# Performance work log

Measured on AMD Instinct MI355X. Metric: run time of the kernel, lower is better.

The kernel has to match this reference:

```python
import jax, jax.numpy as jnp
import numpy as np
from jax import lax

G, K, KS = 4, 16, 3            # stripes, latents per stripe, support kernel
TEMP, TOPK_RATIO, GATE, EPS = 0.125, 0.125, 0.05, 1e-6


def _l2norm(v):
    # F.normalize(p=2, dim=-1): divide by max(norm, 1e-12)
    return v / jnp.maximum(jnp.linalg.norm(v, axis=-1, keepdims=True), 1e-12)


def _avg_pool3(x):
    # 3x3 avg pool, stride 1, pad 1, count_include_pad=True (torch default)
    s = lax.reduce_window(x, 0.0, lax.add, (1, 1, KS, KS), (1, 1, 1, 1),
                          [(0, 0), (0, 0), (KS // 2, KS // 2), (KS // 2, KS // 2)])
    return s / float(KS * KS)


def setup_inputs() -> dict:
    key = jax.random.key(0)
    k1, k2 = jax.random.split(key)
    x = jax.random.normal(k1, (64, 256, 64, 44), dtype=jnp.float32)
    latent_basis = jax.random.normal(k2, (G, K, 256), dtype=jnp.float32) * 0.05
    return {"x": x, "latent_basis": latent_basis}


def reference(x, latent_basis):
    n, c, h, w = x.shape
    hs = h // G
    # 'n c (g hs) w -> (n g) c hs w'
    sf = x.reshape(n, c, G, hs, w).transpose(0, 2, 1, 3, 4).reshape(n * G, c, hs, w)
    support_feat = _avg_pool3(sf)
    feat_flat = sf.reshape(n, G, c, hs * w).transpose(0, 1, 3, 2)          # n g p c
    supp_flat = support_feat.reshape(n, G, c, hs * w).transpose(0, 1, 3, 2)  # n g p c
    # active mask from detached energy
    e = jnp.mean(lax.stop_gradient(sf) ** 2, axis=1)                       # [n*G, hs, w]
    e = e / jnp.maximum(jnp.max(e, axis=(-2, -1), keepdims=True), EPS)
    am = (e > GATE).astype(jnp.float32)
    fb = (e > 0).astype(jnp.float32)
    use_fb = jnp.sum(am, axis=(-2, -1), keepdims=True) <= 0
    am = jnp.where(use_fb, fb, am).reshape(n, G, hs * w)                   # n g p
    # routing
    sfn = _l2norm(supp_flat)
    lb = _l2norm(latent_basis)                                             # g k c
    logits = jnp.einsum('ngpc,gkc->ngpk', sfn, lb) / TEMP
    route = jax.nn.softmax(logits, axis=-1)
    supp = route * am[..., None]                                           # n g p k
    pw = supp / jnp.maximum(jnp.sum(supp, axis=2, keepdims=True), EPS)
    tokens = jnp.einsum('ngpk,ngpc->ngkc', pw, feat_flat)                  # n g k c
    tokens = tokens.transpose(0, 3, 1, 2).reshape(n, c, G * K)             # n c (g k)
    # presence via top-k over positions
    p = supp.shape[2]
    topk = max(1, min(p, int(p * TOPK_RATIO)))
    vals = lax.top_k(supp.transpose(0, 1, 3, 2), topk)[0]                  # n g k topk
    pres = jnp.mean(vals, axis=-1).reshape(n, G * K)
    pres = pres / jnp.maximum(jnp.sum(pres, axis=1, keepdims=True), EPS)
    return tokens, pres
```

## Files before the change

kernel.cpp:

```cpp
#include <hip/hip_runtime.h>
#include <cstdint>


#define C_ 256
#define W_ 44
#define P_ 704
#define CH_STRIDE 2816
#define NB_STRIDE 720896
#define TOPK_ 88
#define GATE_ 0.05f
#define EPS_ 1e-6f

#define DPP_WAVE_SHL1 0x130
#define DPP_WAVE_SHR1 0x138
__device__ __forceinline__ float dpp_from_left(float v) {
  return __int_as_float(__builtin_amdgcn_update_dpp(
      0, __float_as_int(v), DPP_WAVE_SHR1, 0xF, 0xF, true));
}
__device__ __forceinline__ float dpp_from_right(float v) {
  return __int_as_float(__builtin_amdgcn_update_dpp(
      0, __float_as_int(v), DPP_WAVE_SHL1, 0xF, 0xF, true));
}

__global__ __launch_bounds__(256) void k_norm_basis(const float* __restrict__ lb,
                                                    float* __restrict__ lbn) {
  int gk = blockIdx.x;
  int t = threadIdx.x;
  float v = lb[gk * 256 + t];
  float ss = v * v;
  #pragma unroll
  for (int off = 32; off >= 1; off >>= 1) ss += __shfl_xor(ss, off);
  __shared__ float red[4];
  if ((t & 63) == 0) red[t >> 6] = ss;
  __syncthreads();
  float tot = red[0] + red[1] + red[2] + red[3];
  float scale = 1.f / fmaxf(sqrtf(tot), 1e-12f);
  int g = gk >> 4, k = gk & 15;
  lbn[((g * 256 + t) << 4) + k] = v * scale;
}

#define LOAD_GRP(Pm, P0, Pp, cbase)                                    \
  { _Pragma("unroll")                                                  \
    for (int j_ = 0; j_ < 4; j_++) {                                   \
      const size_t o_ = (size_t)((cbase) + j_) * CH_STRIDE;            \
      Pm[j_] = xm[o_]; P0[j_] = xb[o_]; Pp[j_] = xp[o_];               \
    } }

#define CONS_GRP(Pm, P0, Pp, cbase)                                    \
  { _Pragma("unroll")                                                  \
    for (int j_ = 0; j_ < 4; j_++) {                                   \
      float a  = act ? P0[j_] : 0.f;                                   \
      float am_ = (act && hm) ? Pm[j_] : 0.f;                          \
      float ap_ = (act && hp) ? Pp[j_] : 0.f;                          \
      float vs = am_ + a + ap_;                                        \
      float lf = dpp_from_left(vs);                                    \
      float rt = dpp_from_right(vs);                                   \
      float win = lf + vs + rt;                                        \
      pw2 = fmaf(win, win, pw2);                                       \
      sq  = fmaf(a, a, sq);                                            \
      const int co_ = __builtin_amdgcn_readfirstlane(((cbase) + j_) << 4); \
      const float4* wp4 = (const float4*)(lbb + co_);                  \
      float4 w0 = wp4[0], w1 = wp4[1], w2 = wp4[2], w3 = wp4[3];       \
      rawdot[0]  = fmaf(a, w0.x, rawdot[0]);  rawdot[1]  = fmaf(a, w0.y, rawdot[1]);  \
      rawdot[2]  = fmaf(a, w0.z, rawdot[2]);  rawdot[3]  = fmaf(a, w0.w, rawdot[3]);  \
      rawdot[4]  = fmaf(a, w1.x, rawdot[4]);  rawdot[5]  = fmaf(a, w1.y, rawdot[5]);  \
      rawdot[6]  = fmaf(a, w1.z, rawdot[6]);  rawdot[7]  = fmaf(a, w1.w, rawdot[7]);  \
      rawdot[8]  = fmaf(a, w2.x, rawdot[8]);  rawdot[9]  = fmaf(a, w2.y, rawdot[9]);  \
      rawdot[10] = fmaf(a, w2.z, rawdot[10]); rawdot[11] = fmaf(a, w2.w, rawdot[11]); \
      rawdot[12] = fmaf(a, w3.x, rawdot[12]); rawdot[13] = fmaf(a, w3.y, rawdot[13]); \
      rawdot[14] = fmaf(a, w3.z, rawdot[14]); rawdot[15] = fmaf(a, w3.w, rawdot[15]); \
    } }

__global__ __launch_bounds__(256, 4) void k_route_dot(const float* __restrict__ x,
                                                      const float* __restrict__ lbn,
                                                      float* __restrict__ pd0,
                                                      float* __restrict__ pd1,
                                                      float* __restrict__ sqpw) {
  const int tid = threadIdx.x;
  const int wq = tid >> 6;
  const int l = tid & 63;
  const bool act = (l < 44);
  const int bid = blockIdx.x;
  const int s = bid >> 3;
  const int rem = bid & 7;
  const int q = rem >> 1, half = rem & 1;
  const int w = q * 4 + wq;
  const int n = s >> 2, g = s & 3;
  const int p = w * 44 + l;

  const int lsafe = act ? l : 0;
  const float* xb = x + (size_t)n * NB_STRIDE + (size_t)(half * 128) * CH_STRIDE
                      + (g * 16 + w) * 44 + lsafe;
  const float* xm = xb + ((w > 0)  ? -44 : 0);
  const float* xp = xb + ((w < 15) ?  44 : 0);
  const bool hm = (w > 0), hp = (w < 15);

  const float* lbb = lbn + (g << 12) + (half << 11);

  float rawdot[16];
  #pragma unroll
  for (int k = 0; k < 16; k++) rawdot[k] = 0.f;
  float sq = 0.f, pw2 = 0.f;

  float Avm[4], Av0[4], Avp[4];
  float Bvm[4], Bv0[4], Bvp[4];

  LOAD_GRP(Avm, Av0, Avp, 0)
  for (int c = 0; c < 128; c += 8) {
    LOAD_GRP(Bvm, Bv0, Bvp, c + 4)
    CONS_GRP(Avm, Av0, Avp, c)
    if (c + 8 < 128) { LOAD_GRP(Avm, Av0, Avp, c + 8) }
    CONS_GRP(Bvm, Bv0, Bvp, c + 4)
  }

  if (act) {
    float* dst = (half ? pd1 : pd0) + (size_t)s * 11264 + p * 16;
    #pragma unroll
    for (int kq = 0; kq < 4; kq++)
      ((float4*)dst)[kq] = make_float4(rawdot[kq*4+0], rawdot[kq*4+1],
                                       rawdot[kq*4+2], rawdot[kq*4+3]);
    *(float2*)(sqpw + ((size_t)(s * 2 + half) * 704 + p) * 2) = make_float2(sq, pw2);
  }
}

__global__ __launch_bounds__(1024) void k_route_fin(const float* __restrict__ pd0,
                                                    const float* __restrict__ pd1,
                                                    const float* __restrict__ sqpw,
                                                    float* __restrict__ supp_pk,
                                                    float* __restrict__ invden_ws,
                                                    float* __restrict__ presraw) {
  __shared__ float rsl[11264];
  __shared__ uint32_t hist_l[16 * 256];
  __shared__ float redA[16];
  __shared__ float redB[16];
  __shared__ float redM[2];
  __shared__ float red2[16 * 16];

  const int tid = threadIdx.x;
  const int w = tid >> 6;
  const int l = tid & 63;
  const bool act = (l < 44);
  const int s = blockIdx.x;
  const int p = w * 44 + l;

  float sq = 0.f, pw2 = 0.f;
  if (act) {
    const float4* a0 = (const float4*)(pd0 + (size_t)s * 11264 + p * 16);
    const float4* a1 = (const float4*)(pd1 + (size_t)s * 11264 + p * 16);
    #pragma unroll
    for (int kq = 0; kq < 4; kq++) {
      float4 u = a0[kq], v = a1[kq];
      rsl[(kq*4+0) * 704 + p] = u.x + v.x;
      rsl[(kq*4+1) * 704 + p] = u.y + v.y;
      rsl[(kq*4+2) * 704 + p] = u.z + v.z;
      rsl[(kq*4+3) * 704 + p] = u.w + v.w;
    }
    float2 s0 = *(const float2*)(sqpw + ((size_t)(s * 2 + 0) * 704 + p) * 2);
    float2 s1 = *(const float2*)(sqpw + ((size_t)(s * 2 + 1) * 704 + p) * 2);
    sq = s0.x + s1.x; pw2 = s0.y + s1.y;
  }
  __syncthreads();

  float pd[16];
  #pragma unroll
  for (int k = 0; k < 16; k++) pd[k] = 0.f;
  if (act) {
    #pragma unroll
    for (int dy = -1; dy <= 1; dy++) {
      int yy = w + dy;
      if (yy < 0 || yy > 15) continue;
      #pragma unroll
      for (int dx = -1; dx <= 1; dx++) {
        int xx = l + dx;
        if (xx < 0 || xx > 43) continue;
        int pp = yy * 44 + xx;
        #pragma unroll
        for (int k = 0; k < 16; k++) pd[k] += rsl[k * 704 + pp];
      }
    }
  }

  float e_raw = sq * (1.f / 256.f);
  float m = e_raw;
  #pragma unroll
  for (int off = 32; off >= 1; off >>= 1) m = fmaxf(m, __shfl_xor(m, off));
  if (l == 0) redA[w] = m;
  __syncthreads();
  if (tid == 0) {
    float mm = redA[0];
    for (int w2 = 1; w2 < 16; w2++) mm = fmaxf(mm, redA[w2]);
    redM[0] = mm;
  }
  __syncthreads();
  float M = fmaxf(redM[0], EPS_);
  float e = e_raw / M;
  float am = (e > GATE_) ? 1.f : 0.f;
  float fb = (e_raw > 0.f) ? 1.f : 0.f;
  float a = am;
  #pragma unroll
  for (int off = 32; off >= 1; off >>= 1) a += __shfl_xor(a, off);
  if (l == 0) redB[w] = a;
  __syncthreads();
  if (tid == 0) {
    float sm = 0.f;
    for (int w2 = 0; w2 < 16; w2++) sm += redB[w2];
    redM[1] = sm;
  }
  __syncthreads();
  if (redM[1] <= 0.f) am = fb;

  float pnorm = sqrtf(pw2) * (1.f / 9.f);
  float invn = 1.f / fmaxf(pnorm, 1e-12f);
  float scl = invn * (8.f / 9.f);
  float li[16];
  float mx = -1e30f;
  #pragma unroll
  for (int k = 0; k < 16; k++) { li[k] = pd[k] * scl; mx = fmaxf(mx, li[k]); }
  float ssum = 0.f;
  #pragma unroll
  for (int k = 0; k < 16; k++) { li[k] = __expf(li[k] - mx); ssum += li[k]; }
  float rs2 = am / ssum;
  float supp[16];
  #pragma unroll
  for (int k = 0; k < 16; k++) supp[k] = li[k] * rs2;

  if (act) {
    float* spk = supp_pk + ((size_t)s * 704 + p) * 16;
    #pragma unroll
    for (int kq = 0; kq < 4; kq++)
      ((float4*)spk)[kq] = make_float4(supp[kq*4+0], supp[kq*4+1],
                                       supp[kq*4+2], supp[kq*4+3]);
  }

  #pragma unroll
  for (int k = 0; k < 16; k++) {
    float v2 = act ? supp[k] : 0.f;
    #pragma unroll
    for (int off = 32; off >= 1; off >>= 1) v2 += __shfl_xor(v2, off);
    if (l == 0) red2[w * 16 + k] = v2;
  }
  __syncthreads();
  if (tid < 16) {
    float den = 0.f;
    for (int w2 = 0; w2 < 16; w2++) den += red2[w2 * 16 + tid];
    invden_ws[s * 16 + tid] = 1.f / fmaxf(den, EPS_);
  }

  if (act) {
    #pragma unroll
    for (int k = 0; k < 16; k++) rsl[k * 704 + p] = supp[k];
  }
  __syncthreads();

  {
    const int k = w;
    uint32_t key[11];
    #pragma unroll
    for (int j = 0; j < 11; j++)
      key[j] = __float_as_uint(rsl[k * 704 + l + 64 * j]);
    uint32_t* h = &hist_l[w * 256];
    uint32_t prefix = 0, remaining = TOPK_;
    #pragma unroll
    for (int b = 3; b >= 0; b--) {
      const int shift = b * 8;
      *(uint4*)&h[l * 4] = make_uint4(0u, 0u, 0u, 0u);
      uint32_t mhi = (b == 3) ? 0u : (0xFFFFFFFFu << (shift + 8));
      #pragma unroll
      for (int j = 0; j < 11; j++)
        if ((key[j] & mhi) == (prefix & mhi))
          atomicAdd(&h[(key[j] >> shift) & 255u], 1u);
      uint4 bn = *(uint4*)&h[l * 4];
      uint32_t T = bn.x + bn.y + bn.z + bn.w;
      uint32_t inc = T;
      #pragma unroll
      for (int off = 1; off < 64; off <<= 1) {
        uint32_t o = (uint32_t)__shfl_down((int)inc, off);
        if (l + off < 64) inc += o;
      }
      uint32_t excl = inc - T;
      uint32_t g3 = excl + bn.w, g2 = g3 + bn.z, g1 = g2 + bn.y, g0 = g1 + bn.x;
      uint32_t pk = 0u;
      if (g0 >= remaining && g1 < remaining) pk = ((uint32_t)(4*l+0) << 16) | (remaining - g1);
      if (g1 >= remaining && g2 < remaining) pk = ((uint32_t)(4*l+1) << 16) | (remaining - g2);
      if (g2 >= remaining && g3 < remaining) pk = ((uint32_t)(4*l+2) << 16) | (remaining - g3);
      if (g3 >= remaining && excl < remaining) pk = ((uint32_t)(4*l+3) << 16) | (remaining - excl);
      #pragma unroll
      for (int off = 32; off >= 1; off >>= 1) pk |= (uint32_t)__shfl_xor((int)pk, off);
      prefix |= ((pk >> 16) & 255u) << shift;
      remaining = pk & 0xFFFFu;
    }
    float tf = __uint_as_float(prefix);
    float sgt = 0.f; uint32_t cgt = 0u;
    #pragma unroll
    for (int j = 0; j < 11; j++)
      if (key[j] > prefix) { sgt += __uint_as_float(key[j]); cgt++; }
    #pragma unroll
    for (int off = 32; off >= 1; off >>= 1) {
      sgt += __shfl_xor(sgt, off);
      cgt += (uint32_t)__shfl_xor((int)cgt, off);
    }
    if (l == 0)
      presraw[s * 16 + k] = (sgt + (float)(TOPK_ - cgt) * tf) * (1.f / (float)TOPK_);
  }
}

__global__ __launch_bounds__(512, 4) void k_tokens(const float* __restrict__ x,
                                                   const float* __restrict__ supp_pk,
                                                   const float* __restrict__ invden,
                                                   float* __restrict__ out) {
  __shared__ float xl[4096];
  const int tid = threadIdx.x;
  const int bid = blockIdx.x;
  const int s = bid >> 1, chalf = bid & 1;
  const int n = s >> 2, g = s & 3;
  const int cl = tid & 127;
  const int q = tid >> 7;
  const int sblk = s * (704 * 16);

  const float* xs = x + (size_t)n * NB_STRIDE + (size_t)(chalf * 128) * CH_STRIDE + g * P_;

  const int li0 = tid, li1 = tid + 512;
  const int lc0 = li0 >> 3, lj0 = li0 & 7;
  const int lc1 = li1 >> 3, lj1 = li1 & 7;
  const float* gp0 = xs + (size_t)lc0 * CH_STRIDE + lj0 * 4;
  const float* gp1 = xs + (size_t)lc1 * CH_STRIDE + lj1 * 4;
  const int wo0 = lc0 * 32 + ((lj0 * 4) ^ ((lc0 & 7) * 4));
  const int wo1 = lc1 * 32 + ((lj1 * 4) ^ ((lc1 & 7) * 4));

  const int sw = (cl & 7) * 4;
  const int rbase = cl * 32;

  float acc[16];
  #pragma unroll
  for (int k = 0; k < 16; k++) acc[k] = 0.f;

  float4 r0 = *(const float4*)gp0;
  float4 r1 = *(const float4*)gp1;
  *(float4*)&xl[wo0] = r0;
  *(float4*)&xl[wo1] = r1;
  __syncthreads();

  for (int tt = 0; tt < 22; tt++) {
    const int p0 = tt * 32;
    float4 n0, n1;
    if (tt < 21) {
      n0 = *(const float4*)(gp0 + p0 + 32);
      n1 = *(const float4*)(gp1 + p0 + 32);
    }

    #pragma unroll
    for (int jj = 0; jj < 8; jj += 4) {
      const int pp0 = q * 8 + jj;
      float4 xv = *(const float4*)&xl[rbase + (pp0 ^ sw)];
      float xa[4] = {xv.x, xv.y, xv.z, xv.w};
      #pragma unroll
      for (int dj = 0; dj < 4; dj++) {
        int uofs = __builtin_amdgcn_readfirstlane(sblk + (p0 + pp0 + dj) * 16);
        const float4* sp = (const float4*)(supp_pk + uofs);
        float4 s0 = sp[0], s1 = sp[1], s2 = sp[2], s3 = sp[3];
        float a = xa[dj];
        acc[0]  += a * s0.x; acc[1]  += a * s0.y; acc[2]  += a * s0.z; acc[3]  += a * s0.w;
        acc[4]  += a * s1.x; acc[5]  += a * s1.y; acc[6]  += a * s1.z; acc[7]  += a * s1.w;
        acc[8]  += a * s2.x; acc[9]  += a * s2.y; acc[10] += a * s2.z; acc[11] += a * s2.w;
        acc[12] += a * s3.x; acc[13] += a * s3.y; acc[14] += a * s3.z; acc[15] += a * s3.w;
      }
    }

    __syncthreads();
    if (tt < 21) {
      *(float4*)&xl[wo0] = n0;
      *(float4*)&xl[wo1] = n1;
      __syncthreads();
    }
  }

  if (q >= 2) {
    float* dst = &xl[((q - 2) * 128 + cl) * 16];
    #pragma unroll
    for (int kq = 0; kq < 4; kq++)
      ((float4*)dst)[kq] = make_float4(acc[kq*4], acc[kq*4+1], acc[kq*4+2], acc[kq*4+3]);
  }
  __syncthreads();
  if (q < 2) {
    const float* src = &xl[(q * 128 + cl) * 16];
    #pragma unroll
    for (int k = 0; k < 16; k++) acc[k] += src[k];
  }
  __syncthreads();
  if (q == 1) {
    float* dst = &xl[cl * 16];
    #pragma unroll
    for (int kq = 0; kq < 4; kq++)
      ((float4*)dst)[kq] = make_float4(acc[kq*4], acc[kq*4+1], acc[kq*4+2], acc[kq*4+3]);
  }
  __syncthreads();
  if (q == 0) {
    const float* src = &xl[cl * 16];
    float* op = out + ((size_t)(n * 256 + chalf * 128 + cl) * 64) + g * 16;
    #pragma unroll
    for (int kq = 0; kq < 4; kq++) {
      int u = __builtin_amdgcn_readfirstlane(s * 16 + kq * 4);
      const float4 iv = *(const float4*)(invden + u);
      float4 o;
      o.x = (acc[kq*4+0] + src[kq*4+0]) * iv.x;
      o.y = (acc[kq*4+1] + src[kq*4+1]) * iv.y;
      o.z = (acc[kq*4+2] + src[kq*4+2]) * iv.z;
      o.w = (acc[kq*4+3] + src[kq*4+3]) * iv.w;
      ((float4*)op)[kq] = o;
    }
  }
}

__global__ __launch_bounds__(64) void k_pres(const float* __restrict__ presraw,
                                             float* __restrict__ out) {
  const int n = blockIdx.x, t = threadIdx.x;
  float v = presraw[n * 64 + t];
  float ssum = v;
  #pragma unroll
  for (int off = 32; off >= 1; off >>= 1) ssum += __shfl_xor(ssum, off);
  out[1048576 + n * 64 + t] = v / fmaxf(ssum, EPS_);
}

extern "C" void kernel_launch(void* const* d_in, const int* in_sizes, int n_in,
                              void* d_out, int out_size, void* d_ws, size_t ws_size,
                              hipStream_t stream) {
  (void)in_sizes; (void)n_in; (void)out_size; (void)ws_size;
  const float* x  = (const float*)d_in[0];
  const float* lb = (const float*)d_in[1];
  float* out = (float*)d_out;
  float* ws = (float*)d_ws;
  float* lbn_ws     = ws;
  float* invden_ws  = ws + 16384;
  float* presraw_ws = ws + 20480;
  float* supp_kp_ws = ws + 24576;
  float* supp_pk_ws = ws + 2908160;
  float* sqpw_ws    = out;

  k_norm_basis<<<64, 256, 0, stream>>>(lb, lbn_ws);
  k_route_dot<<<2048, 256, 0, stream>>>(x, lbn_ws, supp_kp_ws, supp_pk_ws, sqpw_ws);
  k_route_fin<<<256, 1024, 0, stream>>>(supp_kp_ws, supp_pk_ws, sqpw_ws,
                                        supp_pk_ws, invden_ws, presraw_ws);
  k_tokens<<<512, 512, 0, stream>>>(x, supp_pk_ws, invden_ws, out);
  k_pres<<<64, 64, 0, stream>>>(presraw_ws, out);
}
```

Baseline: 345.7 us.

## Pack positions densely across wave lanes in route_dot with halo lanes

Changes k_route_dot's lane-to-position mapping. Each 64-lane wave now covers 62 consecutive flattened positions plus halo lanes, instead of one 44-wide row with 20 idle lanes. Row boundaries inside a wave are handled by masking the DPP neighbour values at columns 0 and 43, and the grid shrinks from 2048 to 1536 blocks. The aim is to cut wasted lanes and the redundant loads and FMAs they cause. In exchange it adds per-lane modulo arithmetic and unaligned loads that straddle rows, and the last wave is only partly used.

```diff
diff --git a/kernel.cpp b/kernel.cpp
--- a/kernel.cpp
+++ b/kernel.cpp
@@ -53,8 +53,8 @@
       float am_ = (act && hm) ? Pm[j_] : 0.f;                          \
       float ap_ = (act && hp) ? Pp[j_] : 0.f;                          \
       float vs = am_ + a + ap_;                                        \
-      float lf = dpp_from_left(vs);                                    \
-      float rt = dpp_from_right(vs);                                   \
+      float lf = dpp_from_left(vs);  lf = coln0  ? lf : 0.f;           \
+      float rt = dpp_from_right(vs); rt = coln43 ? rt : 0.f;           \
       float win = lf + vs + rt;                                        \
       pw2 = fmaf(win, win, pw2);                                       \
       sq  = fmaf(a, a, sq);                                            \
@@ -79,21 +79,25 @@
   const int tid = threadIdx.x;
   const int wq = tid >> 6;
   const int l = tid & 63;
-  const bool act = (l < 44);
   const int bid = blockIdx.x;
-  const int s = bid >> 3;
-  const int rem = bid & 7;
+  const int s = bid / 6;
+  const int rem = bid % 6;
   const int q = rem >> 1, half = rem & 1;
-  const int w = q * 4 + wq;
+  const int wv = q * 4 + wq;
   const int n = s >> 2, g = s & 3;
-  const int p = w * 44 + l;
-
-  const int lsafe = act ? l : 0;
+  const int p = wv * 62 + l;
+  const int psafe = (p <= 703) ? p : 703;
+  const int col = psafe % 44;
+  const bool act = (p <= 703);
+  const bool own = (l >= 1 && l <= 62 && p <= 703) || (wv == 0 && l == 0);
+  const bool hm = (psafe >= 44);
+  const bool hp = (psafe <= 659);
+  const bool coln0 = (col != 0), coln43 = (col != 43);
+
   const float* xb = x + (size_t)n * NB_STRIDE + (size_t)(half * 128) * CH_STRIDE
-                      + (g * 16 + w) * 44 + lsafe;
-  const float* xm = xb + ((w > 0)  ? -44 : 0);
-  const float* xp = xb + ((w < 15) ?  44 : 0);
-  const bool hm = (w > 0), hp = (w < 15);
+                      + g * 704 + psafe;
+  const float* xm = xb + (hm ? -44 : 0);
+  const float* xp = xb + (hp ?  44 : 0);
 
   const float* lbb = lbn + (g << 12) + (half << 11);
 
@@ -113,13 +117,13 @@
     CONS_GRP(Bvm, Bv0, Bvp, c + 4)
   }
 
-  if (act) {
-    float* dst = (half ? pd1 : pd0) + (size_t)s * 11264 + p * 16;
+  if (own) {
+    float* dst = (half ? pd1 : pd0) + (size_t)s * 11264 + psafe * 16;
     #pragma unroll
     for (int kq = 0; kq < 4; kq++)
       ((float4*)dst)[kq] = make_float4(rawdot[kq*4+0], rawdot[kq*4+1],
                                        rawdot[kq*4+2], rawdot[kq*4+3]);
-    *(float2*)(sqpw + ((size_t)(s * 2 + half) * 704 + p) * 2) = make_float2(sq, pw2);
+    *(float2*)(sqpw + ((size_t)(s * 2 + half) * 704 + psafe) * 2) = make_float2(sq, pw2);
   }
 }
 
@@ -437,7 +441,7 @@
   float* sqpw_ws    = out;
 
   k_norm_basis<<<64, 256, 0, stream>>>(lb, lbn_ws);
-  k_route_dot<<<2048, 256, 0, stream>>>(x, lbn_ws, supp_kp_ws, supp_pk_ws, sqpw_ws);
+  k_route_dot<<<1536, 256, 0, stream>>>(x, lbn_ws, supp_kp_ws, supp_pk_ws, sqpw_ws);
   k_route_fin<<<256, 1024, 0, stream>>>(supp_kp_ws, supp_pk_ws, sqpw_ws,
                                         supp_pk_ws, invden_ws, presraw_ws);
   k_tokens<<<512, 512, 0, stream>>>(x, supp_pk_ws, invden_ws, out);
```

New measurement: 345.3 us. Within noise of the previous version (-0.1%).

## Register-block four rows per wave in route_dot to reuse halo loads

Applied to the files above, without the earlier changes.

Each wave now computes four consecutive image rows instead of one, loading six rows per channel (the four rows plus one halo row on each side) instead of three loads per output row. This removes the redundant vertical-halo reloads and amortizes each basis-weight load over four rows. The grid shrinks from 2048 to 512 blocks, and per-thread accumulators grow to 64 dot products, so launch bounds are relaxed to 2 waves/SIMD. The risks are higher register pressure, lower occupancy and fewer blocks to hide memory latency.

```diff
diff --git a/kernel.cpp b/kernel.cpp
--- a/kernel.cpp
+++ b/kernel.cpp
@@ -39,39 +39,40 @@
   lbn[((g * 256 + t) << 4) + k] = v * scale;
 }
 
-#define LOAD_GRP(Pm, P0, Pp, cbase)                                    \
-  { _Pragma("unroll")                                                  \
+#define LOAD6(R, cbase)                                                \
+  { const size_t o_ = (size_t)(cbase) * CH_STRIDE;                     \
+    R[0] = rp0[o_]; R[1] = rp1[o_]; R[2] = rp2[o_];                    \
+    R[3] = rp3[o_]; R[4] = rp4[o_]; R[5] = rp5[o_]; }
+
+#define CONS6(R, cbase)                                                \
+  { const int co_ = __builtin_amdgcn_readfirstlane((cbase) << 4);      \
+    const float4* wp4 = (const float4*)(lbb + co_);                    \
+    float4 w0 = wp4[0], w1 = wp4[1], w2 = wp4[2], w3 = wp4[3];         \
+    _Pragma("unroll")                                                  \
     for (int j_ = 0; j_ < 4; j_++) {                                   \
-      const size_t o_ = (size_t)((cbase) + j_) * CH_STRIDE;            \
-      Pm[j_] = xm[o_]; P0[j_] = xb[o_]; Pp[j_] = xp[o_];               \
-    } }
-
-#define CONS_GRP(Pm, P0, Pp, cbase)                                    \
-  { _Pragma("unroll")                                                  \
-    for (int j_ = 0; j_ < 4; j_++) {                                   \
-      float a  = act ? P0[j_] : 0.f;                                   \
-      float am_ = (act && hm) ? Pm[j_] : 0.f;                          \
-      float ap_ = (act && hp) ? Pp[j_] : 0.f;                          \
+      float a  = act ? R[j_ + 1] : 0.f;                                \
+      bool hmj = (j_ > 0) || hmw;                                      \
+      bool hpj = (j_ < 3) || hpw;                                      \
+      float am_ = (act && hmj) ? R[j_] : 0.f;                          \
+      float ap_ = (act && hpj) ? R[j_ + 2] : 0.f;                      \
       float vs = am_ + a + ap_;                                        \
       float lf = dpp_from_left(vs);                                    \
       float rt = dpp_from_right(vs);                                   \
       float win = lf + vs + rt;                                        \
-      pw2 = fmaf(win, win, pw2);                                       \
-      sq  = fmaf(a, a, sq);                                            \
-      const int co_ = __builtin_amdgcn_readfirstlane(((cbase) + j_) << 4); \
-      const float4* wp4 = (const float4*)(lbb + co_);                  \
-      float4 w0 = wp4[0], w1 = wp4[1], w2 = wp4[2], w3 = wp4[3];       \
-      rawdot[0]  = fmaf(a, w0.x, rawdot[0]);  rawdot[1]  = fmaf(a, w0.y, rawdot[1]);  \
-      rawdot[2]  = fmaf(a, w0.z, rawdot[2]);  rawdot[3]  = fmaf(a, w0.w, rawdot[3]);  \
-      rawdot[4]  = fmaf(a, w1.x, rawdot[4]);  rawdot[5]  = fmaf(a, w1.y, rawdot[5]);  \
-      rawdot[6]  = fmaf(a, w1.z, rawdot[6]);  rawdot[7]  = fmaf(a, w1.w, rawdot[7]);  \
-      rawdot[8]  = fmaf(a, w2.x, rawdot[8]);  rawdot[9]  = fmaf(a, w2.y, rawdot[9]);  \
-      rawdot[10] = fmaf(a, w2.z, rawdot[10]); rawdot[11] = fmaf(a, w2.w, rawdot[11]); \
-      rawdot[12] = fmaf(a, w3.x, rawdot[12]); rawdot[13] = fmaf(a, w3.y, rawdot[13]); \
-      rawdot[14] = fmaf(a, w3.z, rawdot[14]); rawdot[15] = fmaf(a, w3.w, rawdot[15]); \
+      pw2[j_] = fmaf(win, win, pw2[j_]);                               \
+      sq[j_]  = fmaf(a, a, sq[j_]);                                    \
+      float* rd = &rawdot[j_][0];                                      \
+      rd[0]  = fmaf(a, w0.x, rd[0]);  rd[1]  = fmaf(a, w0.y, rd[1]);   \
+      rd[2]  = fmaf(a, w0.z, rd[2]);  rd[3]  = fmaf(a, w0.w, rd[3]);   \
+      rd[4]  = fmaf(a, w1.x, rd[4]);  rd[5]  = fmaf(a, w1.y, rd[5]);   \
+      rd[6]  = fmaf(a, w1.z, rd[6]);  rd[7]  = fmaf(a, w1.w, rd[7]);   \
+      rd[8]  = fmaf(a, w2.x, rd[8]);  rd[9]  = fmaf(a, w2.y, rd[9]);   \
+      rd[10] = fmaf(a, w2.z, rd[10]); rd[11] = fmaf(a, w2.w, rd[11]);  \
+      rd[12] = fmaf(a, w3.x, rd[12]); rd[13] = fmaf(a, w3.y, rd[13]);  \
+      rd[14] = fmaf(a, w3.z, rd[14]); rd[15] = fmaf(a, w3.w, rd[15]);  \
     } }
 
-__global__ __launch_bounds__(256, 4) void k_route_dot(const float* __restrict__ x,
+__global__ __launch_bounds__(256, 2) void k_route_dot(const float* __restrict__ x,
                                                       const float* __restrict__ lbn,
                                                       float* __restrict__ pd0,
                                                       float* __restrict__ pd1,
@@ -81,45 +82,53 @@
   const int l = tid & 63;
   const bool act = (l < 44);
   const int bid = blockIdx.x;
-  const int s = bid >> 3;
-  const int rem = bid & 7;
-  const int q = rem >> 1, half = rem & 1;
-  const int w = q * 4 + wq;
+  const int s = bid >> 1, half = bid & 1;
   const int n = s >> 2, g = s & 3;
-  const int p = w * 44 + l;
+  const int rbase = wq * 4;
+  const bool hmw = (wq > 0);
+  const bool hpw = (wq < 3);
 
   const int lsafe = act ? l : 0;
-  const float* xb = x + (size_t)n * NB_STRIDE + (size_t)(half * 128) * CH_STRIDE
-                      + (g * 16 + w) * 44 + lsafe;
-  const float* xm = xb + ((w > 0)  ? -44 : 0);
-  const float* xp = xb + ((w < 15) ?  44 : 0);
-  const bool hm = (w > 0), hp = (w < 15);
+  const float* xc = x + (size_t)n * NB_STRIDE + (size_t)(half * 128) * CH_STRIDE
+                      + g * 704 + lsafe;
+  const float* rp0 = xc + ((rbase - 1 < 0)  ? 0  : rbase - 1) * 44;
+  const float* rp1 = xc + (rbase + 0) * 44;
+  const float* rp2 = xc + (rbase + 1) * 44;
+  const float* rp3 = xc + (rbase + 2) * 44;
+  const float* rp4 = xc + (rbase + 3) * 44;
+  const float* rp5 = xc + ((rbase + 4 > 15) ? 15 : rbase + 4) * 44;
 
   const float* lbb = lbn + (g << 12) + (half << 11);
 
-  float rawdot[16];
-  #pragma unroll
-  for (int k = 0; k < 16; k++) rawdot[k] = 0.f;
-  float sq = 0.f, pw2 = 0.f;
-
-  float Avm[4], Av0[4], Avp[4];
-  float Bvm[4], Bv0[4], Bvp[4];
-
-  LOAD_GRP(Avm, Av0, Avp, 0)
-  for (int c = 0; c < 128; c += 8) {
-    LOAD_GRP(Bvm, Bv0, Bvp, c + 4)
-    CONS_GRP(Avm, Av0, Avp, c)
-    if (c + 8 < 128) { LOAD_GRP(Avm, Av0, Avp, c + 8) }
-    CONS_GRP(Bvm, Bv0, Bvp, c + 4)
+  float rawdot[4][16];
+  #pragma unroll
+  for (int j = 0; j < 4; j++)
+    #pragma unroll
+    for (int k = 0; k < 16; k++) rawdot[j][k] = 0.f;
+  float sq[4] = {0.f, 0.f, 0.f, 0.f};
+  float pw2[4] = {0.f, 0.f, 0.f, 0.f};
+
+  float A[6], B[6];
+  LOAD6(A, 0)
+  for (int c = 0; c < 128; c += 2) {
+    LOAD6(B, c + 1)
+    CONS6(A, c)
+    if (c + 2 < 128) { LOAD6(A, c + 2) }
+    CONS6(B, c + 1)
   }
 
   if (act) {
-    float* dst = (half ? pd1 : pd0) + (size_t)s * 11264 + p * 16;
-    #pragma unroll
-    for (int kq = 0; kq < 4; kq++)
-      ((float4*)dst)[kq] = make_float4(rawdot[kq*4+0], rawdot[kq*4+1],
-                                       rawdot[kq*4+2], rawdot[kq*4+3]);
-    *(float2*)(sqpw + ((size_t)(s * 2 + half) * 704 + p) * 2) = make_float2(sq, pw2);
+    #pragma unroll
+    for (int j = 0; j < 4; j++) {
+      const int p = (rbase + j) * 44 + l;
+      float* dst = (half ? pd1 : pd0) + (size_t)s * 11264 + p * 16;
+      #pragma unroll
+      for (int kq = 0; kq < 4; kq++)
+        ((float4*)dst)[kq] = make_float4(rawdot[j][kq*4+0], rawdot[j][kq*4+1],
+                                         rawdot[j][kq*4+2], rawdot[j][kq*4+3]);
+      *(float2*)(sqpw + ((size_t)(s * 2 + half) * 704 + p) * 2) =
+          make_float2(sq[j], pw2[j]);
+    }
   }
 }
 
@@ -437,7 +446,7 @@
   float* sqpw_ws    = out;
 
   k_norm_basis<<<64, 256, 0, stream>>>(lb, lbn_ws);
-  k_route_dot<<<2048, 256, 0, stream>>>(x, lbn_ws, supp_kp_ws, supp_pk_ws, sqpw_ws);
+  k_route_dot<<<512, 256, 0, stream>>>(x, lbn_ws, supp_kp_ws, supp_pk_ws, sqpw_ws);
   k_route_fin<<<256, 1024, 0, stream>>>(supp_kp_ws, supp_pk_ws, sqpw_ws,
                                         supp_pk_ws, invden_ws, presraw_ws);
   k_tokens<<<512, 512, 0, stream>>>(x, supp_pk_ws, invden_ws, out);
```

Result: no change. 352.2 us (+1.9%).

## Fuse routing dot-product kernel into routing finalize kernel

Applied to the files above, without the earlier changes.

Merges k_route_dot and k_route_fin into one k_route kernel. Each 1024-thread block now computes the full 256-channel dot products for its stripe and writes them straight to shared memory, with no partial sums sent through global memory. This removes a kernel launch and the global write and re-read of the split-channel partials. In exchange the dot-product phase runs on only 256 blocks instead of 2048, each thread loops over twice as many channels, and the large shared-memory footprint may limit occupancy, so latency hiding could get worse.

```diff
diff --git a/kernel.cpp b/kernel.cpp
--- a/kernel.cpp
+++ b/kernel.cpp
@@ -71,64 +71,11 @@
       rawdot[14] = fmaf(a, w3.z, rawdot[14]); rawdot[15] = fmaf(a, w3.w, rawdot[15]); \
     } }
 
-__global__ __launch_bounds__(256, 4) void k_route_dot(const float* __restrict__ x,
-                                                      const float* __restrict__ lbn,
-                                                      float* __restrict__ pd0,
-                                                      float* __restrict__ pd1,
-                                                      float* __restrict__ sqpw) {
-  const int tid = threadIdx.x;
-  const int wq = tid >> 6;
-  const int l = tid & 63;
-  const bool act = (l < 44);
-  const int bid = blockIdx.x;
-  const int s = bid >> 3;
-  const int rem = bid & 7;
-  const int q = rem >> 1, half = rem & 1;
-  const int w = q * 4 + wq;
-  const int n = s >> 2, g = s & 3;
-  const int p = w * 44 + l;
-
-  const int lsafe = act ? l : 0;
-  const float* xb = x + (size_t)n * NB_STRIDE + (size_t)(half * 128) * CH_STRIDE
-                      + (g * 16 + w) * 44 + lsafe;
-  const float* xm = xb + ((w > 0)  ? -44 : 0);
-  const float* xp = xb + ((w < 15) ?  44 : 0);
-  const bool hm = (w > 0), hp = (w < 15);
-
-  const float* lbb = lbn + (g << 12) + (half << 11);
-
-  float rawdot[16];
-  #pragma unroll
-  for (int k = 0; k < 16; k++) rawdot[k] = 0.f;
-  float sq = 0.f, pw2 = 0.f;
-
-  float Avm[4], Av0[4], Avp[4];
-  float Bvm[4], Bv0[4], Bvp[4];
-
-  LOAD_GRP(Avm, Av0, Avp, 0)
-  for (int c = 0; c < 128; c += 8) {
-    LOAD_GRP(Bvm, Bv0, Bvp, c + 4)
-    CONS_GRP(Avm, Av0, Avp, c)
-    if (c + 8 < 128) { LOAD_GRP(Avm, Av0, Avp, c + 8) }
-    CONS_GRP(Bvm, Bv0, Bvp, c + 4)
-  }
-
-  if (act) {
-    float* dst = (half ? pd1 : pd0) + (size_t)s * 11264 + p * 16;
-    #pragma unroll
-    for (int kq = 0; kq < 4; kq++)
-      ((float4*)dst)[kq] = make_float4(rawdot[kq*4+0], rawdot[kq*4+1],
-                                       rawdot[kq*4+2], rawdot[kq*4+3]);
-    *(float2*)(sqpw + ((size_t)(s * 2 + half) * 704 + p) * 2) = make_float2(sq, pw2);
-  }
-}
-
-__global__ __launch_bounds__(1024) void k_route_fin(const float* __restrict__ pd0,
-                                                    const float* __restrict__ pd1,
-                                                    const float* __restrict__ sqpw,
-                                                    float* __restrict__ supp_pk,
-                                                    float* __restrict__ invden_ws,
-                                                    float* __restrict__ presraw) {
+__global__ __launch_bounds__(1024, 4) void k_route(const float* __restrict__ x,
+                                                   const float* __restrict__ lbn,
+                                                   float* __restrict__ supp_pk,
+                                                   float* __restrict__ invden_ws,
+                                                   float* __restrict__ presraw) {
   __shared__ float rsl[11264];
   __shared__ uint32_t hist_l[16 * 256];
   __shared__ float redA[16];
@@ -140,24 +87,36 @@
   const int w = tid >> 6;
   const int l = tid & 63;
   const bool act = (l < 44);
-  const int s = blockIdx.x;
+  const int s = blockIdx.x, n = s >> 2, g = s & 3;
   const int p = w * 44 + l;
 
+  const int lsafe = act ? l : 0;
+  const float* xb = x + (size_t)n * NB_STRIDE + (g * 16 + w) * 44 + lsafe;
+  const float* xm = xb + ((w > 0)  ? -44 : 0);
+  const float* xp = xb + ((w < 15) ?  44 : 0);
+  const bool hm = (w > 0), hp = (w < 15);
+
+  const float* lbb = lbn + (g << 12);
+
+  float rawdot[16];
+  #pragma unroll
+  for (int k = 0; k < 16; k++) rawdot[k] = 0.f;
   float sq = 0.f, pw2 = 0.f;
+
+  float Avm[4], Av0[4], Avp[4];
+  float Bvm[4], Bv0[4], Bvp[4];
+
+  LOAD_GRP(Avm, Av0, Avp, 0)
+  for (int c = 0; c < 256; c += 8) {
+    LOAD_GRP(Bvm, Bv0, Bvp, c + 4)
+    CONS_GRP(Avm, Av0, Avp, c)
+    if (c + 8 < 256) { LOAD_GRP(Avm, Av0, Avp, c + 8) }
+    CONS_GRP(Bvm, Bv0, Bvp, c + 4)
+  }
+
   if (act) {
-    const float4* a0 = (const float4*)(pd0 + (size_t)s * 11264 + p * 16);
-    const float4* a1 = (const float4*)(pd1 + (size_t)s * 11264 + p * 16);
-    #pragma unroll
-    for (int kq = 0; kq < 4; kq++) {
-      float4 u = a0[kq], v = a1[kq];
-      rsl[(kq*4+0) * 704 + p] = u.x + v.x;
-      rsl[(kq*4+1) * 704 + p] = u.y + v.y;
-      rsl[(kq*4+2) * 704 + p] = u.z + v.z;
-      rsl[(kq*4+3) * 704 + p] = u.w + v.w;
-    }
-    float2 s0 = *(const float2*)(sqpw + ((size_t)(s * 2 + 0) * 704 + p) * 2);
-    float2 s1 = *(const float2*)(sqpw + ((size_t)(s * 2 + 1) * 704 + p) * 2);
-    sq = s0.x + s1.x; pw2 = s0.y + s1.y;
+    #pragma unroll
+    for (int k = 0; k < 16; k++) rsl[k * 704 + p] = rawdot[k];
   }
   __syncthreads();
 
@@ -432,14 +391,10 @@
   float* lbn_ws     = ws;
   float* invden_ws  = ws + 16384;
   float* presraw_ws = ws + 20480;
-  float* supp_kp_ws = ws + 24576;
   float* supp_pk_ws = ws + 2908160;
-  float* sqpw_ws    = out;
 
   k_norm_basis<<<64, 256, 0, stream>>>(lb, lbn_ws);
-  k_route_dot<<<2048, 256, 0, stream>>>(x, lbn_ws, supp_kp_ws, supp_pk_ws, sqpw_ws);
-  k_route_fin<<<256, 1024, 0, stream>>>(supp_kp_ws, supp_pk_ws, sqpw_ws,
-                                        supp_pk_ws, invden_ws, presraw_ws);
+  k_route<<<256, 1024, 0, stream>>>(x, lbn_ws, supp_pk_ws, invden_ws, presraw_ws);
   k_tokens<<<512, 512, 0, stream>>>(x, supp_pk_ws, invden_ws, out);
   k_pres<<<64, 64, 0, stream>>>(presraw_ws, out);
 }
```

After: 333.1 us. 3.6% less time.
